# Optimization experiments

Measured on AMD Instinct MI355X. Metric: run time of the kernel, lower is better.

The kernel has to match this reference:

```python
import jax, jax.numpy as jnp
import numpy as np

B, S, D = 4, 2048, 768
H, R = 12, 8
Dh = D // H


def setup_inputs() -> dict:
    key = jax.random.key(0)
    ks = jax.random.split(key, 12)
    s_in = 1.0 / np.sqrt(D)
    s_r = 1.0 / np.sqrt(R)
    return {
        "x": jax.random.normal(ks[0], (B, S, D), jnp.float32),
        "Wq0": jax.random.normal(ks[1], (D, D), jnp.float32) * s_in,
        "Aq": jax.random.normal(ks[2], (D, R), jnp.float32) * s_in,
        "Bq": jax.random.normal(ks[3], (R, D), jnp.float32) * s_r,
        "Wk0": jax.random.normal(ks[4], (D, D), jnp.float32) * s_in,
        "Ak": jax.random.normal(ks[5], (D, R), jnp.float32) * s_in,
        "Bk": jax.random.normal(ks[6], (R, D), jnp.float32) * s_r,
        "Wv0": jax.random.normal(ks[7], (D, D), jnp.float32) * s_in,
        "Av": jax.random.normal(ks[8], (D, R), jnp.float32) * s_in,
        "Bv": jax.random.normal(ks[9], (R, D), jnp.float32) * s_r,
        "Wo": jax.random.normal(ks[10], (D, D), jnp.float32) * s_in,
        "bo": jnp.zeros((D,), jnp.float32),
    }


def _lora(x, W0, A, Bm):
    # x @ W0 + (x @ A) @ B  -- low-rank adapter on frozen W0
    return x @ W0 + (x @ A) @ Bm


def _split_heads(t):
    # [B,S,D] -> [B,H,S,Dh]
    return t.reshape(B, S, H, Dh).transpose(0, 2, 1, 3)


def reference(x, Wq0, Aq, Bq, Wk0, Ak, Bk, Wv0, Av, Bv, Wo, bo):
    q = _split_heads(_lora(x, Wq0, Aq, Bq))
    k = _split_heads(_lora(x, Wk0, Ak, Bk))
    v = _split_heads(_lora(x, Wv0, Av, Bv))
    scale = 1.0 / jnp.sqrt(jnp.asarray(Dh, x.dtype))
    scores = jnp.einsum("bhqd,bhkd->bhqk", q, k) * scale  # [B,H,S,S]
    weights = jax.nn.softmax(scores, axis=-1)
    attn = jnp.einsum("bhqk,bhkd->bhqd", weights, v)
    concat = attn.transpose(0, 2, 1, 3).reshape(B, S, D)
    return concat @ Wo + bo
```

## Files before the change

### kernel.cpp

```cpp
#include <hip/hip_runtime.h>
#include <hip/hip_bf16.h>


typedef unsigned short ushort_t;
typedef __bf16 bf16x8 __attribute__((ext_vector_type(8)));
typedef float f32x4 __attribute__((ext_vector_type(4)));
typedef float f32x16 __attribute__((ext_vector_type(16)));
typedef unsigned short ushort8 __attribute__((ext_vector_type(8)));
typedef unsigned short ushort4_t __attribute__((ext_vector_type(4)));
typedef unsigned int uint4v __attribute__((ext_vector_type(4)));
typedef __attribute__((address_space(1))) unsigned int gu32;
typedef __attribute__((address_space(3))) unsigned int lu32;

__device__ __forceinline__ unsigned short f2bf(float f) {
  unsigned int u = __builtin_bit_cast(unsigned int, f);
  u += 0x7fffu + ((u >> 16) & 1u);
  return (unsigned short)(u >> 16);
}

__device__ __forceinline__ void gld_lds16(const void* g, void* s) {
  __builtin_amdgcn_global_load_lds((gu32*)(unsigned long long)g,
                                   (lu32*)(unsigned int)(unsigned long long)s,
                                   16, 0, 0);
}

__device__ __forceinline__ f32x4 mfma16(bf16x8 a, bf16x8 b, f32x4 c) {
  return __builtin_amdgcn_mfma_f32_16x16x32_bf16(a, b, c, 0, 0, 0);
}

__device__ __forceinline__ f32x16 mfma32(bf16x8 a, bf16x8 b, f32x16 c) {
  return __builtin_amdgcn_mfma_f32_32x32x16_bf16(a, b, c, 0, 0, 0);
}

__device__ __forceinline__ unsigned int cvtpk(float a, float b) {
  unsigned int r;
  asm("v_cvt_pk_bf16_f32 %0, %1, %2" : "=v"(r) : "v"(a), "v"(b));
  return r;
}

__global__ __launch_bounds__(256) void prep_and_cast(
    const float* __restrict__ x,
    const float* __restrict__ Wq0, const float* __restrict__ Aq, const float* __restrict__ Bq,
    const float* __restrict__ Wk0, const float* __restrict__ Ak, const float* __restrict__ Bk,
    const float* __restrict__ Wv0, const float* __restrict__ Av, const float* __restrict__ Bv,
    const float* __restrict__ Wo,
    ushort_t* __restrict__ xb, ushort_t* __restrict__ WeffT, ushort_t* __restrict__ WoT)
{
  const int tid = threadIdx.x;
  const int bx = blockIdx.x;
  if (bx < 3072) {
    long i = (long)bx * 256 + tid;
    const float4* xp = (const float4*)x;
    float4 a = xp[i * 2], c = xp[i * 2 + 1];
    ushort8 rv;
    rv[0] = f2bf(a.x); rv[1] = f2bf(a.y); rv[2] = f2bf(a.z); rv[3] = f2bf(a.w);
    rv[4] = f2bf(c.x); rv[5] = f2bf(c.y); rv[6] = f2bf(c.z); rv[7] = f2bf(c.w);
    *(ushort8*)&xb[i * 8] = rv;
    return;
  }
  __shared__ float tile[32][33];
  __shared__ float tA[32][8];
  __shared__ float tB[8][32];
  const int bb = bx - 3072;
  const int mat = bb / 576, inner = bb % 576;
  const int kt = inner / 24, nt = inner % 24;
  const int k0 = kt * 32, n0 = nt * 32;
  const float* W0 = (mat == 0) ? Wq0 : (mat == 1) ? Wk0 : (mat == 2) ? Wv0 : Wo;
  const float* Am = (mat == 0) ? Aq : (mat == 1) ? Ak : (mat == 2) ? Av : nullptr;
  const float* Bm = (mat == 0) ? Bq : (mat == 1) ? Bk : (mat == 2) ? Bv : nullptr;
#pragma unroll
  for (int i = 0; i < 4; i++) {
    int rr = i * 8 + (tid >> 5), c = tid & 31;
    tile[rr][c] = W0[(k0 + rr) * 768 + n0 + c];
  }
  if (Am) {
    tA[tid >> 3][tid & 7] = Am[(k0 + (tid >> 3)) * 8 + (tid & 7)];
    tB[tid >> 5][tid & 31] = Bm[(tid >> 5) * 768 + n0 + (tid & 31)];
  }
  __syncthreads();
#pragma unroll
  for (int i = 0; i < 4; i++) {
    int kk = tid & 31;
    int nn = i * 8 + (tid >> 5);
    float val = tile[kk][nn];
    if (Am) {
#pragma unroll
      for (int rr = 0; rr < 8; rr++) val += tA[kk][rr] * tB[rr][nn];
    }
    int n = n0 + nn, kg = k0 + kk;
    if (mat < 3) WeffT[((long)mat * 768 + n) * 768 + kg] = f2bf(val);
    else         WoT[(long)n * 768 + kg] = f2bf(val);
  }
}

template <int MODE>
__global__ __launch_bounds__(256) void gemm_bt(
    const ushort_t* __restrict__ A, const ushort_t* __restrict__ Bt,
    ushort_t* __restrict__ q, ushort_t* __restrict__ kf, ushort_t* __restrict__ vf,
    float* __restrict__ out, const float* __restrict__ bo)
{
  constexpr int K = 768;
  constexpr int NT = K / 64;
  __shared__ __align__(16) ushort_t As[2][128 * 64];
  __shared__ __align__(16) ushort_t Bs[2][128 * 64];
  const int tid = threadIdx.x;
  const int l = tid & 63, w = tid >> 6;
  const int wm = w >> 1, wn = w & 1;
  const int lr = l & 15, lg = l >> 4;
  const long rowBase = (long)blockIdx.x * 128;
  const long colBase = (long)blockIdx.y * 128;
  f32x4 acc[4][4] = {};

  int soff[4];
#pragma unroll
  for (int i = 0; i < 4; i++) {
    int ci = i * 256 + tid, r = ci >> 3, c = ci & 7;
    soff[i] = r * K + ((c ^ (r & 7)) * 8);
  }
  int rdoff[2];
#pragma unroll
  for (int ks = 0; ks < 2; ks++) rdoff[ks] = ((ks * 4 + lg) ^ (lr & 7)) * 8;

  const ushort_t* Abase = A + rowBase * K;
  const ushort_t* Bbase = Bt + colBase * K;

  auto STAGE = [&](int t, int bi) {
    const ushort_t* ap = Abase + t * 64;
    const ushort_t* bp = Bbase + t * 64;
#pragma unroll
    for (int i = 0; i < 4; i++)
      gld_lds16(ap + soff[i], &As[bi][(i * 256 + tid) * 8]);
#pragma unroll
    for (int i = 0; i < 4; i++)
      gld_lds16(bp + soff[i], &Bs[bi][(i * 256 + tid) * 8]);
  };

  STAGE(0, 0);

  for (int t = 0; t < NT; t++) {
    const int cur = t & 1;
    if (t + 1 < NT) {
      STAGE(t + 1, cur ^ 1);
      asm volatile("s_waitcnt vmcnt(8)" ::: "memory");
    } else {
      asm volatile("s_waitcnt vmcnt(0)" ::: "memory");
    }
    __builtin_amdgcn_s_barrier();
#pragma unroll
    for (int ks = 0; ks < 2; ks++) {
      bf16x8 af[4], bf[4];
#pragma unroll
      for (int m = 0; m < 4; m++)
        af[m] = *(const bf16x8*)&As[cur][(wm * 64 + m * 16 + lr) * 64 + rdoff[ks]];
#pragma unroll
      for (int n = 0; n < 4; n++)
        bf[n] = *(const bf16x8*)&Bs[cur][(wn * 64 + n * 16 + lr) * 64 + rdoff[ks]];
#pragma unroll
      for (int m = 0; m < 4; m++)
#pragma unroll
        for (int n = 0; n < 4; n++)
          acc[m][n] = mfma16(af[m], bf[n], acc[m][n]);
    }
    asm volatile("" ::: "memory");
    __builtin_amdgcn_s_barrier();
  }

  if (MODE == 0) {
    const int mat = (int)(colBase / 768);
    __syncthreads();
    ushort_t* myscr = (w < 2) ? &As[0][w * 4096] : &Bs[0][(w - 2) * 4096];
    if (mat == 2) {
      const long cb = colBase - 1536;
#pragma unroll
      for (int m = 0; m < 4; m++) {
        int sp0 = m * 16 + ((lg & 1) << 3) + ((lg >> 1) << 2);
#pragma unroll
        for (int n = 0; n < 4; n++) {
          int lcol = n * 16 + lr;
          int ch = (sp0 >> 3) ^ (lcol & 7);
          ushort4_t pk;
#pragma unroll
          for (int r = 0; r < 4; r++) pk[r] = f2bf(acc[m][n][r]);
          *(ushort4_t*)&myscr[lcol * 64 + ch * 8 + (sp0 & 7)] = pk;
        }
      }
      asm volatile("s_waitcnt lgkmcnt(0)" ::: "memory");
      const long sB = rowBase + wm * 64;
      const long bI = sB >> 11, t = (sB & 2047) >> 6;
      const int hh = (int)((cb + wn * 64) >> 6);
      ushort_t* vfb = vf + ((bI * 12 + hh) * 32 + t) * 4096;
#pragma unroll
      for (int ks = 0; ks < 4; ks++)
#pragma unroll
        for (int half = 0; half < 2; half++) {
          int row = half * 32 + (l >> 1);
          int ch = (ks * 2 + (l & 1)) ^ (row & 7);
          ushort8 vv = *(const ushort8*)&myscr[row * 64 + ch * 8];
          *(ushort8*)&vfb[ks * 1024 + half * 512 + l * 8] = vv;
        }
    } else if (mat == 1) {
      const long cb = colBase - 768;
#pragma unroll
      for (int m = 0; m < 4; m++)
#pragma unroll
        for (int n = 0; n < 4; n++)
#pragma unroll
          for (int r = 0; r < 4; r++) {
            int lrow = m * 16 + lg * 4 + r, lcol = n * 16 + lr;
            int ch = (lcol >> 3) ^ (lrow & 7);
            myscr[lrow * 64 + ch * 8 + (lcol & 7)] = f2bf(acc[m][n][r]);
          }
      asm volatile("s_waitcnt lgkmcnt(0)" ::: "memory");
      const long sB = rowBase + wm * 64;
      const long bI = sB >> 11, t = (sB & 2047) >> 6;
      const int hh = (int)((cb + wn * 64) >> 6);
      ushort_t* kfb = kf + ((bI * 12 + hh) * 32 + t) * 4096;
#pragma unroll
      for (int ks = 0; ks < 4; ks++)
#pragma unroll
        for (int half = 0; half < 2; half++) {
          int row = half * 32 + (l >> 1);
          int ch = (ks * 2 + (l & 1)) ^ (row & 7);
          ushort8 vv = *(const ushort8*)&myscr[row * 64 + ch * 8];
          *(ushort8*)&kfb[ks * 1024 + half * 512 + l * 8] = vv;
        }
    } else {
      const float scl = 0.125f * 1.4426950408889634f;
#pragma unroll
      for (int m = 0; m < 4; m++)
#pragma unroll
        for (int n = 0; n < 4; n++)
#pragma unroll
          for (int r = 0; r < 4; r++) {
            int lrow = m * 16 + lg * 4 + r, lcol = n * 16 + lr;
            int ch = (lcol >> 3) ^ (lrow & 7);
            myscr[lrow * 64 + ch * 8 + (lcol & 7)] = f2bf(acc[m][n][r] * scl);
          }
      asm volatile("s_waitcnt lgkmcnt(0)" ::: "memory");
      const long cg = colBase + wn * 64;
#pragma unroll
      for (int it = 0; it < 8; it++) {
        int rl = (l >> 3) + it * 8;
        int ch = (l & 7) ^ (rl & 7);
        ushort8 vv = *(const ushort8*)&myscr[rl * 64 + ch * 8];
        *(ushort8*)&q[(rowBase + wm * 64 + rl) * 768 + cg + (l & 7) * 8] = vv;
      }
    }
  } else {
#pragma unroll
    for (int m = 0; m < 4; m++)
#pragma unroll
      for (int n = 0; n < 4; n++) {
        long col = colBase + wn * 64 + n * 16 + lr;
        float bv = bo[col];
#pragma unroll
        for (int r = 0; r < 4; r++) {
          long row = rowBase + wm * 64 + m * 16 + lg * 4 + r;
          out[row * 768 + col] = acc[m][n][r] + bv;
        }
      }
  }
}

__global__ __launch_bounds__(256) void attn_fwd(
    const ushort_t* __restrict__ Q, const ushort_t* __restrict__ Kf,
    const ushort_t* __restrict__ Vf, ushort_t* __restrict__ O)
{
  constexpr int D = 768, S = 2048;
  const int tid = threadIdx.x;
  const int l = tid & 63, w = tid >> 6;
  const int q32 = l & 31, hi = l >> 5;
  const int i = blockIdx.x;
  const int xcd = i & 7, j = i >> 3;
  const int bh = xcd * 6 + (j >> 4);
  const int q0 = (j & 15) * 128;
  const int b = bh / 12, h = bh % 12;

  const ushort_t* kbase = Kf + ((long)bh * 32) * 4096 + q32 * 16 + hi * 8;
  const ushort_t* vbase = Vf + ((long)bh * 32) * 4096 + q32 * 16 + hi * 8;

  bf16x8 qf[4];
  {
    const ushort_t* qrow = Q + (long)(b * S + q0 + w * 32 + q32) * D + h * 64 + hi * 8;
#pragma unroll
    for (int ks = 0; ks < 4; ks++) qf[ks] = *(const bf16x8*)&qrow[ks * 16];
  }

  bf16x8 ones;
#pragma unroll
  for (int e = 0; e < 8; e++) ones[e] = (__bf16)1.0f;

  f32x16 oA = {}, oB = {}, osum = {};

  bf16x8 k0[4], k1[4], v0[4], v1[4];
#pragma unroll
  for (int ks = 0; ks < 4; ks++) {
    k0[ks] = *(const bf16x8*)&kbase[ks * 1024];
    k1[ks] = *(const bf16x8*)&kbase[ks * 1024 + 512];
    v0[ks] = *(const bf16x8*)&vbase[ks * 1024];
    v1[ks] = *(const bf16x8*)&vbase[ks * 1024 + 512];
  }

  for (int kt = 0; kt < 32; kt++) {
    const ushort_t* knext = kbase + (kt + 1) * 4096;
    const ushort_t* vnext = vbase + (kt + 1) * 4096;

    f32x16 s0 = {}, s1 = {};
    __builtin_amdgcn_s_setprio(1);
#pragma unroll
    for (int ks = 0; ks < 4; ks++) {
      s0 = mfma32(k0[ks], qf[ks], s0);
      s1 = mfma32(k1[ks], qf[ks], s1);
    }
    __builtin_amdgcn_s_setprio(0);
    if (kt + 1 < 32) {
#pragma unroll
      for (int ks = 0; ks < 4; ks++) {
        k0[ks] = *(const bf16x8*)&knext[ks * 1024];
        k1[ks] = *(const bf16x8*)&knext[ks * 1024 + 512];
      }
    }

    unsigned int pw[16];
#pragma unroll
    for (int u = 0; u < 8; u++) {
      float a0 = __builtin_amdgcn_exp2f(s0[2 * u]);
      float a1 = __builtin_amdgcn_exp2f(s0[2 * u + 1]);
      pw[u] = cvtpk(a0, a1);
    }
#pragma unroll
    for (int u = 0; u < 8; u++) {
      float a0 = __builtin_amdgcn_exp2f(s1[2 * u]);
      float a1 = __builtin_amdgcn_exp2f(s1[2 * u + 1]);
      pw[8 + u] = cvtpk(a0, a1);
    }

    __builtin_amdgcn_s_setprio(1);
#pragma unroll
    for (int ks = 0; ks < 4; ks++) {
      uint4v w4 = {pw[4 * ks], pw[4 * ks + 1], pw[4 * ks + 2], pw[4 * ks + 3]};
      bf16x8 pa = __builtin_bit_cast(bf16x8, w4);
      oA = mfma32(pa, v0[ks], oA);
      oB = mfma32(pa, v1[ks], oB);
      osum = mfma32(pa, ones, osum);
    }
    __builtin_amdgcn_s_setprio(0);
    if (kt + 1 < 32) {
#pragma unroll
      for (int ks = 0; ks < 4; ks++) {
        v0[ks] = *(const bf16x8*)&vnext[ks * 1024];
        v1[ks] = *(const bf16x8*)&vnext[ks * 1024 + 512];
      }
    }
  }

#pragma unroll
  for (int reg = 0; reg < 16; reg++) {
    int row = (reg & 3) + 8 * (reg >> 2) + 4 * hi;
    float inv = 1.0f / osum[reg];
    long base = ((long)b * S + q0 + w * 32 + row) * D + h * 64 + q32;
    O[base] = f2bf(oA[reg] * inv);
    O[base + 32] = f2bf(oB[reg] * inv);
  }
}

extern "C" void kernel_launch(void* const* d_in, const int* in_sizes, int n_in,
                              void* d_out, int out_size, void* d_ws, size_t ws_size,
                              hipStream_t stream)
{
  const float* x   = (const float*)d_in[0];
  const float* Wq0 = (const float*)d_in[1];
  const float* Aq  = (const float*)d_in[2];
  const float* Bq  = (const float*)d_in[3];
  const float* Wk0 = (const float*)d_in[4];
  const float* Ak  = (const float*)d_in[5];
  const float* Bk  = (const float*)d_in[6];
  const float* Wv0 = (const float*)d_in[7];
  const float* Av  = (const float*)d_in[8];
  const float* Bv  = (const float*)d_in[9];
  const float* Wo  = (const float*)d_in[10];
  const float* bo  = (const float*)d_in[11];
  float* out = (float*)d_out;

  char* ws = (char*)d_ws;
  const long SZ = 8192L * 768 * 2;
  ushort_t* xb    = (ushort_t*)(ws);
  ushort_t* Qb    = (ushort_t*)(ws + SZ);
  ushort_t* Kf    = (ushort_t*)(ws + 2 * SZ);
  ushort_t* Vf    = (ushort_t*)(ws + 3 * SZ);
  ushort_t* At    = (ushort_t*)(ws + 4 * SZ);
  ushort_t* WeffT = (ushort_t*)(ws + 5 * SZ);
  ushort_t* WoT   = (ushort_t*)(ws + 5 * SZ + 2304L * 768 * 2);

  hipLaunchKernelGGL(prep_and_cast, dim3(3072 + 2304), dim3(256), 0, stream,
                     x, Wq0, Aq, Bq, Wk0, Ak, Bk, Wv0, Av, Bv, Wo, xb, WeffT, WoT);
  hipLaunchKernelGGL((gemm_bt<0>), dim3(64, 18), dim3(256), 0, stream,
                     xb, WeffT, Qb, Kf, Vf, (float*)nullptr, (const float*)nullptr);
  hipLaunchKernelGGL(attn_fwd, dim3(768), dim3(256), 0, stream, Qb, Kf, Vf, At);
  hipLaunchKernelGGL((gemm_bt<1>), dim3(64, 6), dim3(256), 0, stream,
                     At, WoT, (ushort_t*)nullptr, (ushort_t*)nullptr, (ushort_t*)nullptr,
                     out, bo);
}
```

Before: 157.6 us.

## Stage K/V tiles through double-buffered LDS via async global-to-LDS loads

In the attention kernel, each wave used to load its own K/V fragments from global memory straight into registers, so all four waves fetched the same data. Now the block cooperatively copies each 4096-element K and V tile into a double-buffered LDS area using global_load_lds, prefetching the next tile while computing on the current one, and waves read their fragments from LDS. This cuts redundant global/L2 traffic by the number of waves and frees registers. In exchange it adds two barriers per iteration, LDS read latency, and a wrap-around prefetch of tile 0 on the last iteration.

```diff
diff --git a/kernel.cpp b/kernel.cpp
--- a/kernel.cpp
+++ b/kernel.cpp
@@ -267,6 +267,8 @@
     const ushort_t* __restrict__ Vf, ushort_t* __restrict__ O)
 {
   constexpr int D = 768, S = 2048;
+  __shared__ __align__(16) ushort_t Ks[2][4096];
+  __shared__ __align__(16) ushort_t Vs[2][4096];
   const int tid = threadIdx.x;
   const int l = tid & 63, w = tid >> 6;
   const int q32 = l & 31, hi = l >> 5;
@@ -276,8 +278,8 @@
   const int q0 = (j & 15) * 128;
   const int b = bh / 12, h = bh % 12;
 
-  const ushort_t* kbase = Kf + ((long)bh * 32) * 4096 + q32 * 16 + hi * 8;
-  const ushort_t* vbase = Vf + ((long)bh * 32) * 4096 + q32 * 16 + hi * 8;
+  const ushort_t* kslab = Kf + ((long)bh * 32) * 4096;
+  const ushort_t* vslab = Vf + ((long)bh * 32) * 4096;
 
   bf16x8 qf[4];
   {
@@ -292,34 +294,40 @@
 
   f32x16 oA = {}, oB = {}, osum = {};
 
-  bf16x8 k0[4], k1[4], v0[4], v1[4];
-#pragma unroll
-  for (int ks = 0; ks < 4; ks++) {
-    k0[ks] = *(const bf16x8*)&kbase[ks * 1024];
-    k1[ks] = *(const bf16x8*)&kbase[ks * 1024 + 512];
-    v0[ks] = *(const bf16x8*)&vbase[ks * 1024];
-    v1[ks] = *(const bf16x8*)&vbase[ks * 1024 + 512];
-  }
+  const int fro = q32 * 16 + hi * 8;
+
+  auto STAGE = [&](int kt, int bi) {
+    const ushort_t* kp = kslab + (long)kt * 4096;
+    const ushort_t* vp = vslab + (long)kt * 4096;
+#pragma unroll
+    for (int it = 0; it < 2; it++)
+      gld_lds16(kp + (it * 256 + tid) * 8, &Ks[bi][(it * 256 + tid) * 8]);
+#pragma unroll
+    for (int it = 0; it < 2; it++)
+      gld_lds16(vp + (it * 256 + tid) * 8, &Vs[bi][(it * 256 + tid) * 8]);
+  };
+
+  STAGE(0, 0);
 
   for (int kt = 0; kt < 32; kt++) {
-    const ushort_t* knext = kbase + (kt + 1) * 4096;
-    const ushort_t* vnext = vbase + (kt + 1) * 4096;
+    const int cur = kt & 1;
+    STAGE((kt + 1) & 31, cur ^ 1);
+    asm volatile("s_waitcnt vmcnt(4)" ::: "memory");
+    __builtin_amdgcn_s_barrier();
+
+    const ushort_t* ksb = &Ks[cur][0];
+    const ushort_t* vsb = &Vs[cur][0];
 
     f32x16 s0 = {}, s1 = {};
     __builtin_amdgcn_s_setprio(1);
 #pragma unroll
     for (int ks = 0; ks < 4; ks++) {
-      s0 = mfma32(k0[ks], qf[ks], s0);
-      s1 = mfma32(k1[ks], qf[ks], s1);
+      bf16x8 kf0 = *(const bf16x8*)&ksb[ks * 1024 + fro];
+      bf16x8 kf1 = *(const bf16x8*)&ksb[ks * 1024 + 512 + fro];
+      s0 = mfma32(kf0, qf[ks], s0);
+      s1 = mfma32(kf1, qf[ks], s1);
     }
     __builtin_amdgcn_s_setprio(0);
-    if (kt + 1 < 32) {
-#pragma unroll
-      for (int ks = 0; ks < 4; ks++) {
-        k0[ks] = *(const bf16x8*)&knext[ks * 1024];
-        k1[ks] = *(const bf16x8*)&knext[ks * 1024 + 512];
-      }
-    }
 
     unsigned int pw[16];
 #pragma unroll
@@ -340,18 +348,16 @@
     for (int ks = 0; ks < 4; ks++) {
       uint4v w4 = {pw[4 * ks], pw[4 * ks + 1], pw[4 * ks + 2], pw[4 * ks + 3]};
       bf16x8 pa = __builtin_bit_cast(bf16x8, w4);
-      oA = mfma32(pa, v0[ks], oA);
-      oB = mfma32(pa, v1[ks], oB);
+      bf16x8 vf0 = *(const bf16x8*)&vsb[ks * 1024 + fro];
+      bf16x8 vf1 = *(const bf16x8*)&vsb[ks * 1024 + 512 + fro];
+      oA = mfma32(pa, vf0, oA);
+      oB = mfma32(pa, vf1, oB);
       osum = mfma32(pa, ones, osum);
     }
     __builtin_amdgcn_s_setprio(0);
-    if (kt + 1 < 32) {
-#pragma unroll
-      for (int ks = 0; ks < 4; ks++) {
-        v0[ks] = *(const bf16x8*)&vnext[ks * 1024];
-        v1[ks] = *(const bf16x8*)&vnext[ks * 1024 + 512];
-      }
-    }
+
+    asm volatile("" ::: "memory");
+    __builtin_amdgcn_s_barrier();
   }
 
 #pragma unroll
```

After: 150.4 us. 1.05x faster.
